# Kernel optimization log

Measured on AMD Instinct MI355X. Metric: run time of the kernel, lower is better.

Reference implementation:

```python
import jax, jax.numpy as jnp
import numpy as np
import math

BS, QLEN, DIM, NHEADS = 2, 2048, 1024, 16
HEAD = DIM // NHEADS

def linear(x, w, b):
    # torch nn.Linear: y = x @ w.T + b, w: [out, in]
    return x @ w.T + b

def setup_inputs() -> dict:
    key = jax.random.key(0)
    ks = jax.random.split(key, 6)
    s = 1.0 / math.sqrt(DIM)
    return {
        "input": jax.random.normal(ks[0], (BS * QLEN, DIM), jnp.float32),
        "mask": jnp.zeros((BS, 1, 1, QLEN), jnp.float32),
        "q_w": jax.random.normal(ks[1], (DIM, DIM), jnp.float32) * s,
        "q_b": jnp.zeros((DIM,), jnp.float32),
        "k_w": jax.random.normal(ks[2], (DIM, DIM), jnp.float32) * s,
        "k_b": jnp.zeros((DIM,), jnp.float32),
        "v_w": jax.random.normal(ks[3], (DIM, DIM), jnp.float32) * s,
        "v_b": jnp.zeros((DIM,), jnp.float32),
        "o_w": jax.random.normal(ks[4], (DIM, DIM), jnp.float32) * s,
        "o_b": jnp.zeros((DIM,), jnp.float32),
        "bs": BS,
        "qlen": QLEN,
    }

def reference(input, mask, q_w, q_b, k_w, k_b, v_w, v_b, o_w, o_b, bs, qlen):
    dim = input.shape[-1]
    n_heads = NHEADS
    dph = dim // n_heads

    def split_heads(x):  # [bs*qlen, dim] -> [bs, h, qlen, dph]
        return x.reshape(bs, qlen, n_heads, dph).transpose(0, 2, 1, 3)

    q = split_heads(linear(input, q_w, q_b)) * (1.0 / math.sqrt(dph))
    k = split_heads(linear(input, k_w, k_b))
    v = split_heads(linear(input, v_w, v_b))

    scores = jnp.einsum('bhqd,bhkd->bhqk', q, k) + mask
    weights = jax.nn.softmax(scores.astype(jnp.float32), axis=-1).astype(scores.dtype)
    # dropout: eval mode (training=False) -> identity
    context = jnp.einsum('bhqk,bhkd->bhqd', weights, v)
    context = context.transpose(0, 2, 1, 3).reshape(bs * qlen, dim)
    return linear(context, o_w, o_b)
```

## Files before the change

### kernel.cpp

```cpp
#include <hip/hip_runtime.h>
#include <hip/hip_bf16.h>

typedef __bf16 bf16;
typedef __attribute__((ext_vector_type(8))) __bf16 bf16x8;
typedef __attribute__((ext_vector_type(4))) __bf16 bf16x4;
typedef __attribute__((ext_vector_type(4))) float f32x4;

#define GLOAD_LDS16(g, l) __builtin_amdgcn_global_load_lds( \
    (const __attribute__((address_space(1))) void*)(g),     \
    (__attribute__((address_space(3))) void*)(l), 16, 0, 0)

#if __has_builtin(__builtin_amdgcn_exp2f)
#define EXP2F(x) __builtin_amdgcn_exp2f(x)
#else
#define EXP2F(x) exp2f(x)
#endif

constexpr int MTOT = 4096;
constexpr int DIMC = 1024;
constexpr int QL   = 2048;
constexpr int NH   = 16;
constexpr int HD   = 64;
constexpr float LOG2E = 1.44269504088896340736f;

__global__ __launch_bounds__(256) void prep_cvt(
    const float* __restrict__ x,  const float* __restrict__ qw,
    const float* __restrict__ kw, const float* __restrict__ vw,
    const float* __restrict__ ow, const float* __restrict__ mask,
    bf16* __restrict__ Xb, bf16* __restrict__ Wq, bf16* __restrict__ Wk,
    bf16* __restrict__ Wv, bf16* __restrict__ Wo, bf16* __restrict__ Mexp)
{
  const long long bid = blockIdx.x;
  if (bid >= 8192) {
    const int off = (int)(bid - 8192) * 1024 + threadIdx.x * 4;
    float4 f = *reinterpret_cast<const float4*>(mask + off);
    bf16x4 v;
    v[0] = (bf16)exp2f(f.x * LOG2E); v[1] = (bf16)exp2f(f.y * LOG2E);
    v[2] = (bf16)exp2f(f.z * LOG2E); v[3] = (bf16)exp2f(f.w * LOG2E);
    *reinterpret_cast<bf16x4*>(Mexp + off) = v;
    return;
  }
  const long long i = (bid * 256 + threadIdx.x) * 4;
  const long long nX = (long long)MTOT * DIMC;
  const long long nW = (long long)DIMC * DIMC;
  const float* src; bf16* dst; long long off;
  if      (i < nX)          { src = x;  dst = Xb; off = i; }
  else if (i < nX + nW)     { src = qw; dst = Wq; off = i - nX; }
  else if (i < nX + 2*nW)   { src = kw; dst = Wk; off = i - nX - nW; }
  else if (i < nX + 3*nW)   { src = vw; dst = Wv; off = i - nX - 2*nW; }
  else                      { src = ow; dst = Wo; off = i - nX - 3*nW; }
  float4 f = *reinterpret_cast<const float4*>(src + off);
  bf16x4 v;
  v[0] = (bf16)f.x; v[1] = (bf16)f.y; v[2] = (bf16)f.z; v[3] = (bf16)f.w;
  *reinterpret_cast<bf16x4*>(dst + off) = v;
}

__global__ __launch_bounds__(128, 2) void gemm_bt(
    const bf16* __restrict__ A,
    const bf16* __restrict__ W0, const bf16* __restrict__ W1, const bf16* __restrict__ W2,
    const float* __restrict__ b0, const float* __restrict__ b1, const float* __restrict__ b2,
    bf16* __restrict__ D0, bf16* __restrict__ D1,
    bf16* __restrict__ VtOut, const bf16* __restrict__ Mexp, float scale0)
{
  __shared__ __align__(16) bf16 SMEM[16384];
  bf16* As = SMEM;
  bf16* Bs = SMEM + 8192;

  const bf16* Bm; const float* bias; bf16* D = nullptr; float scale = 1.f;
  const int z = blockIdx.z;
  if (z == 0)      { Bm = W0; bias = b0; D = D0; scale = scale0; }
  else if (z == 1) { Bm = W1; bias = b1; D = D1; }
  else             { Bm = W2; bias = b2; }

  const int tid  = threadIdx.x;
  const int w    = tid >> 6, lane = tid & 63;
  const int gm0  = blockIdx.x * 128, gn0 = blockIdx.y * 128;
  const int wc   = w * 64;
  const int lr   = lane & 15;
  const int lkB  = (lane >> 4) * 16;
  const int srow = (w << 3) + (lane >> 3);
  const int scolE = (((lane & 7) * 16) ^ (((lane >> 3) & 7) << 4)) >> 1;

  f32x4 acc[8][4] = {};

  for (int kt = 0; kt < DIMC / 64; ++kt) {
    __syncthreads();
    const int k0 = kt * 64;
#pragma unroll
    for (int p = 0; p < 8; ++p) {
      const int r = p * 16 + srow;
      GLOAD_LDS16(A  + (size_t)(gm0 + r) * DIMC + k0 + scolE, &As[(p * 16 + (w << 3)) * 64]);
      GLOAD_LDS16(Bm + (size_t)(gn0 + r) * DIMC + k0 + scolE, &Bs[(p * 16 + (w << 3)) * 64]);
    }
    asm volatile("s_waitcnt vmcnt(0)" ::: "memory");
    __syncthreads();

#pragma unroll
    for (int kk = 0; kk < 2; ++kk) {
      bf16x8 af[8], bfv[4];
#pragma unroll
      for (int mf = 0; mf < 8; ++mf) {
        const int r = mf * 16 + lr;
        const int cE = ((kk * 64 + lkB) ^ ((r & 7) << 4)) >> 1;
        af[mf] = *reinterpret_cast<const bf16x8*>(&As[r * 64 + cE]);
      }
#pragma unroll
      for (int nf = 0; nf < 4; ++nf) {
        const int r = wc + nf * 16 + lr;
        const int cE = ((kk * 64 + lkB) ^ ((r & 7) << 4)) >> 1;
        bfv[nf] = *reinterpret_cast<const bf16x8*>(&Bs[r * 64 + cE]);
      }
#pragma unroll
      for (int mf = 0; mf < 8; ++mf)
#pragma unroll
        for (int nf = 0; nf < 4; ++nf)
          acc[mf][nf] = __builtin_amdgcn_mfma_f32_16x16x32_bf16(af[mf], bfv[nf], acc[mf][nf], 0, 0, 0);
    }
  }

  const int orow = (lane >> 4) * 4;

  if (z == 2) {
    bf16* T = SMEM;
    __syncthreads();
#pragma unroll
    for (int mf = 0; mf < 8; ++mf) {
#pragma unroll
      for (int nf = 0; nf < 4; ++nf) {
        const int cl = wc + nf * 16 + lr;
        const float bv = bias[gn0 + cl];
        const int xx = (cl & 7) << 3;
        const int rl0 = mf * 16 + orow;
        bf16x4 tv;
#pragma unroll
        for (int i = 0; i < 4; ++i) tv[i] = (bf16)(acc[mf][nf][i] + bv);
        *reinterpret_cast<bf16x4*>(&T[cl * 128 + (rl0 ^ xx)]) = tv;
      }
    }
    __syncthreads();
    const int c   = tid;
    const int xx2 = (c & 7) << 3;
    const int cg  = gn0 + c;
    const int bb  = gm0 >> 11;
    const int kvb = gm0 & 2047;
    bf16* vtrow = VtOut + (((size_t)bb * 16 + (cg >> 6)) * 64 + (cg & 63)) * (size_t)QL
                  + kvb;
    const bf16* mrow = Mexp + (size_t)bb * QL + kvb;
    const int st = c & 15;
#pragma unroll
    for (int j = 0; j < 16; ++j) {
      const int jj = (j + st) & 15;
      bf16x8 vv = *reinterpret_cast<const bf16x8*>(&T[c * 128 + ((jj * 8) ^ xx2)]);
      const bf16x8 me = *reinterpret_cast<const bf16x8*>(mrow + jj * 8);
#pragma unroll
      for (int e = 0; e < 8; ++e) vv[e] = (bf16)((float)vv[e] * (float)me[e]);
      *reinterpret_cast<bf16x8*>(vtrow + jj * 8) = vv;
    }
    return;
  }

#pragma unroll
  for (int mf = 0; mf < 8; ++mf) {
#pragma unroll
    for (int nf = 0; nf < 4; ++nf) {
      const int c = gn0 + wc + nf * 16 + lr;
      const float bv = bias[c];
#pragma unroll
      for (int i = 0; i < 4; ++i) {
        const int r = gm0 + mf * 16 + orow + i;
        D[(size_t)r * DIMC + c] = (bf16)((acc[mf][nf][i] + bv) * scale);
      }
    }
  }
}

__global__ __launch_bounds__(256) void gemm_o(
    const bf16* __restrict__ A, const bf16* __restrict__ W,
    const float* __restrict__ bias, float* __restrict__ out)
{
  __shared__ __align__(16) bf16 As[128 * 64];
  __shared__ __align__(16) bf16 Bs[64 * 64];

  const int tid  = threadIdx.x;
  const int w    = tid >> 6, lane = tid & 63;
  const int gm0  = blockIdx.x * 128, gn0 = blockIdx.y * 64;
  const int wr   = (w >> 1) * 64, wc = (w & 1) * 32;
  const int lr   = lane & 15;
  const int lkB  = (lane >> 4) * 16;
  const int srow = (w << 3) + (lane >> 3);
  const int scolE = (((lane & 7) * 16) ^ ((lane >> 3) << 4)) >> 1;

  f32x4 acc[4][2] = {};

  for (int kt = 0; kt < DIMC / 64; ++kt) {
    __syncthreads();
    const int k0 = kt * 64;
#pragma unroll
    for (int p = 0; p < 4; ++p) {
      const int r = p * 32 + srow;
      GLOAD_LDS16(A + (size_t)(gm0 + r) * DIMC + k0 + scolE, &As[(p * 32 + (w << 3)) * 64]);
    }
#pragma unroll
    for (int p = 0; p < 2; ++p) {
      const int r = p * 32 + srow;
      GLOAD_LDS16(W + (size_t)(gn0 + r) * DIMC + k0 + scolE, &Bs[(p * 32 + (w << 3)) * 64]);
    }
    asm volatile("s_waitcnt vmcnt(0)" ::: "memory");
    __syncthreads();

#pragma unroll
    for (int kk = 0; kk < 2; ++kk) {
      bf16x8 af[4], bfv[2];
#pragma unroll
      for (int mf = 0; mf < 4; ++mf) {
        const int r = wr + mf * 16 + lr;
        const int cE = ((kk * 64 + lkB) ^ ((r & 7) << 4)) >> 1;
        af[mf] = *reinterpret_cast<const bf16x8*>(&As[r * 64 + cE]);
      }
#pragma unroll
      for (int nf = 0; nf < 2; ++nf) {
        const int r = wc + nf * 16 + lr;
        const int cE = ((kk * 64 + lkB) ^ ((r & 7) << 4)) >> 1;
        bfv[nf] = *reinterpret_cast<const bf16x8*>(&Bs[r * 64 + cE]);
      }
#pragma unroll
      for (int mf = 0; mf < 4; ++mf)
#pragma unroll
        for (int nf = 0; nf < 2; ++nf)
          acc[mf][nf] = __builtin_amdgcn_mfma_f32_16x16x32_bf16(af[mf], bfv[nf], acc[mf][nf], 0, 0, 0);
    }
  }

  const int orow = (lane >> 4) * 4;
#pragma unroll
  for (int mf = 0; mf < 4; ++mf) {
#pragma unroll
    for (int nf = 0; nf < 2; ++nf) {
      const int c = gn0 + wc + nf * 16 + lr;
      const float bv = bias[c];
#pragma unroll
      for (int i = 0; i < 4; ++i) {
        const int r = gm0 + wr + mf * 16 + orow + i;
        out[(size_t)r * DIMC + c] = acc[mf][nf][i] + bv;
      }
    }
  }
}

__global__ __launch_bounds__(256, 2) void attn_fwd(
    const bf16* __restrict__ Q, const bf16* __restrict__ K, const bf16* __restrict__ Vt,
    const bf16* __restrict__ Mexp, bf16* __restrict__ ctx)
{
  __shared__ __align__(16) bf16 Kls[4 * 4096];
  __shared__ __align__(16) bf16 Vls[4 * 4096];
  __shared__ __align__(16) bf16 Ps[4][2 * 16 * 36];

  const int tid = threadIdx.x, w = tid >> 6, lane = tid & 63;
  const int bid = blockIdx.x;
  const int logical = (bid & 7) * 64 + (bid >> 3);
  const int qt = logical & 15, bh = logical >> 4;
  const int b = bh >> 4, h = bh & 15;
  const size_t rowbase = (size_t)b * QL;
  const int lr = lane & 15, g = lane >> 4;
  const int lkB = g * 16;

  bf16x8 aq[2][2];
#pragma unroll
  for (int s = 0; s < 2; ++s) {
    const bf16* qp = Q + (rowbase + qt * 128 + w * 32 + s * 16 + lr) * DIMC + h * HD + g * 8;
    aq[s][0] = *reinterpret_cast<const bf16x8*>(qp);
    aq[s][1] = *reinterpret_cast<const bf16x8*>(qp + 32);
  }

  int g_row[2], g_colE[2];
#pragma unroll
  for (int s2 = 0; s2 < 2; ++s2) {
    const int ci = s2 * 256 + tid;
    const int row = ci >> 3;
    g_row[s2]  = row;
    g_colE[s2] = (((ci & 7) * 16) ^ ((row & 7) << 4)) >> 1;
  }
  const bf16* Kt0 = K  + rowbase * DIMC + h * HD;
  const bf16* Vt0 = Vt + (size_t)bh * HD * QL;
  const bf16* MexpP = Mexp + rowbase;

#define ATTN_STAGE(tt, bb) do {                                               \
    _Pragma("unroll")                                                         \
    for (int s2 = 0; s2 < 2; ++s2) {                                          \
      GLOAD_LDS16(Kt0 + (size_t)((tt) * 64 + g_row[s2]) * DIMC + g_colE[s2],  \
                  &Kls[(bb) * 4096 + (s2 * 256 + tid) * 8]);                  \
      GLOAD_LDS16(Vt0 + (size_t)g_row[s2] * QL + (tt) * 64 + g_colE[s2],      \
                  &Vls[(bb) * 4096 + (s2 * 256 + tid) * 8]);                  \
    }                                                                         \
  } while (0)

  const f32x4 zf4 = {0.f, 0.f, 0.f, 0.f};

#define QK_COMPUTE(TT, SACC) do {                                             \
    const bf16* Kb = &Kls[((TT) & 3) * 4096];                                 \
    bf16x8 bk0[4], bk1[4];                                                    \
    _Pragma("unroll")                                                         \
    for (int nf = 0; nf < 4; ++nf) {                                          \
      const int r = nf * 16 + lr;                                             \
      const int c0 = ((lkB)      ^ ((r & 7) << 4)) >> 1;                      \
      const int c1 = ((64 + lkB) ^ ((r & 7) << 4)) >> 1;                      \
      bk0[nf] = *reinterpret_cast<const bf16x8*>(&Kb[r * 64 + c0]);           \
      bk1[nf] = *reinterpret_cast<const bf16x8*>(&Kb[r * 64 + c1]);           \
    }                                                                         \
    __builtin_amdgcn_s_setprio(1);                                            \
    _Pragma("unroll")                                                         \
    for (int s = 0; s < 2; ++s)                                               \
      _Pragma("unroll")                                                       \
      for (int nf = 0; nf < 4; ++nf)                                          \
        SACC[s][nf] = __builtin_amdgcn_mfma_f32_16x16x32_bf16(bk0[nf], aq[s][0], zf4, 0, 0, 0); \
    _Pragma("unroll")                                                         \
    for (int s = 0; s < 2; ++s)                                               \
      _Pragma("unroll")                                                       \
      for (int nf = 0; nf < 4; ++nf)                                          \
        SACC[s][nf] = __builtin_amdgcn_mfma_f32_16x16x32_bf16(bk1[nf], aq[s][1], SACC[s][nf], 0, 0, 0); \
    __builtin_amdgcn_s_setprio(0);                                            \
  } while (0)

#define SM_PV_HALF(TT, SC, HALF) do {                                         \
    _Pragma("unroll")                                                         \
    for (int s = 0; s < 2; ++s) {                                             \
      _Pragma("unroll")                                                       \
      for (int nn = 0; nn < 2; ++nn) {                                        \
        const int nf = (HALF) * 2 + nn;                                       \
        const float p0 = EXP2F(SC[s][nf][0]);                                 \
        const float p1 = EXP2F(SC[s][nf][1]);                                 \
        const float p2 = EXP2F(SC[s][nf][2]);                                 \
        const float p3 = EXP2F(SC[s][nf][3]);                                 \
        bf16x4 pv;                                                            \
        pv[0] = (bf16)p0; pv[1] = (bf16)p1; pv[2] = (bf16)p2; pv[3] = (bf16)p3; \
        *reinterpret_cast<bf16x4*>(&Ps[w][s * 576 + lr * 36 + nn * 16 + g * 4]) = pv; \
      }                                                                       \
    }                                                                         \
    const bf16x8 mfrag = *reinterpret_cast<const bf16x8*>(                    \
        MexpP + (TT) * 64 + (HALF) * 32 + g * 8);                             \
    const bf16* Vb = &Vls[((TT) & 3) * 4096];                                 \
    bf16x8 bv[4];                                                             \
    _Pragma("unroll")                                                         \
    for (int df = 0; df < 4; ++df) {                                          \
      const int r = df * 16 + lr;                                             \
      const int cE = (((HALF) * 64 + lkB) ^ ((r & 7) << 4)) >> 1;             \
      bv[df] = *reinterpret_cast<const bf16x8*>(&Vb[r * 64 + cE]);            \
    }                                                                         \
    bf16x8 ap0, ap1;                                                          \
    {                                                                         \
      const bf16x4 lo0 = *reinterpret_cast<const bf16x4*>(&Ps[w][0 * 576 + lr * 36 + g * 8]); \
      const bf16x4 hi0 = *reinterpret_cast<const bf16x4*>(&Ps[w][0 * 576 + lr * 36 + g * 8 + 4]); \
      const bf16x4 lo1 = *reinterpret_cast<const bf16x4*>(&Ps[w][1 * 576 + lr * 36 + g * 8]); \
      const bf16x4 hi1 = *reinterpret_cast<const bf16x4*>(&Ps[w][1 * 576 + lr * 36 + g * 8 + 4]); \
      _Pragma("unroll")                                                       \
      for (int j = 0; j < 4; ++j) {                                           \
        ap0[j] = lo0[j]; ap0[4 + j] = hi0[j];                                 \
        ap1[j] = lo1[j]; ap1[4 + j] = hi1[j];                                 \
      }                                                                       \
    }                                                                         \
    __builtin_amdgcn_s_setprio(1);                                            \
    acc_l[0] = __builtin_amdgcn_mfma_f32_16x16x32_bf16(ap0, mfrag, acc_l[0], 0, 0, 0); \
    acc_l[1] = __builtin_amdgcn_mfma_f32_16x16x32_bf16(ap1, mfrag, acc_l[1], 0, 0, 0); \
    _Pragma("unroll")                                                         \
    for (int df = 0; df < 4; ++df)                                            \
      acc_o[0][df] = __builtin_amdgcn_mfma_f32_16x16x32_bf16(ap0, bv[df], acc_o[0][df], 0, 0, 0); \
    _Pragma("unroll")                                                         \
    for (int df = 0; df < 4; ++df)                                            \
      acc_o[1][df] = __builtin_amdgcn_mfma_f32_16x16x32_bf16(ap1, bv[df], acc_o[1][df], 0, 0, 0); \
    __builtin_amdgcn_s_setprio(0);                                            \
  } while (0)

#define ITER_END() do {                                                       \
    asm volatile("s_waitcnt vmcnt(4) lgkmcnt(0)" ::: "memory");               \
    __builtin_amdgcn_s_barrier();                                             \
    __builtin_amdgcn_sched_barrier(0);                                        \
  } while (0)

  f32x4 acc_l[2] = {};
  f32x4 acc_o[2][4] = {};
  f32x4 sA[2][4], sB[2][4];

  constexpr int NT = QL / 64;

  ATTN_STAGE(0, 0);
  ATTN_STAGE(1, 1);
  ATTN_STAGE(2, 2);
  asm volatile("s_waitcnt vmcnt(8)" ::: "memory");
  __builtin_amdgcn_s_barrier();
  QK_COMPUTE(0, sA);
  ITER_END();

  for (int tt = 0; tt < NT; tt += 2) {
    {
      const int T = tt;
      const int stg = (T + 3 < NT) ? (T + 3) : (NT - 1);
      ATTN_STAGE(stg, (T + 3) & 3);
      QK_COMPUTE(T + 1, sB);
      SM_PV_HALF(T, sA, 0);
      SM_PV_HALF(T, sA, 1);
      ITER_END();
    }
    {
      const int T = tt + 1;
      const int stg = (T + 3 < NT) ? (T + 3) : (NT - 1);
      ATTN_STAGE(stg, (T + 3) & 3);
      if (T + 1 < NT) QK_COMPUTE(T + 1, sA);
      SM_PV_HALF(T, sB, 0);
      SM_PV_HALF(T, sB, 1);
      ITER_END();
    }
  }
#undef ATTN_STAGE
#undef QK_COMPUTE
#undef SM_PV_HALF
#undef ITER_END

#pragma unroll
  for (int s = 0; s < 2; ++s) {
#pragma unroll
    for (int i = 0; i < 4; ++i) {
      const float inv = 1.0f / acc_l[s][i];
      const size_t r = rowbase + qt * 128 + w * 32 + s * 16 + g * 4 + i;
#pragma unroll
      for (int df = 0; df < 4; ++df)
        ctx[r * DIMC + h * HD + df * 16 + lr] = (bf16)(acc_o[s][df][i] * inv);
    }
  }
}

extern "C" void kernel_launch(void* const* d_in, const int* in_sizes, int n_in,
                              void* d_out, int out_size, void* d_ws, size_t ws_size,
                              hipStream_t stream) {
  const float* x    = (const float*)d_in[0];
  const float* mask = (const float*)d_in[1];
  const float* qw = (const float*)d_in[2]; const float* qb = (const float*)d_in[3];
  const float* kw = (const float*)d_in[4]; const float* kb = (const float*)d_in[5];
  const float* vw = (const float*)d_in[6]; const float* vb = (const float*)d_in[7];
  const float* ow = (const float*)d_in[8]; const float* ob = (const float*)d_in[9];
  float* out = (float*)d_out;

  bf16* Xb  = (bf16*)d_ws;
  bf16* Wqb = Xb  + (size_t)MTOT * DIMC;
  bf16* Wkb = Wqb + (size_t)DIMC * DIMC;
  bf16* Wvb = Wkb + (size_t)DIMC * DIMC;
  bf16* Wob = Wvb + (size_t)DIMC * DIMC;
  bf16* Qb  = Wob + (size_t)DIMC * DIMC;
  bf16* Kb  = Qb  + (size_t)MTOT * DIMC;
  bf16* Cb  = Kb  + (size_t)MTOT * DIMC;
  bf16* Vt  = Cb  + (size_t)MTOT * DIMC;
  bf16* Mex = Vt  + (size_t)MTOT * DIMC;

  prep_cvt<<<8196, 256, 0, stream>>>(x, qw, kw, vw, ow, mask,
                                     Xb, Wqb, Wkb, Wvb, Wob, Mex);

  gemm_bt<<<dim3(32, 8, 3), 128, 0, stream>>>(
      Xb, Wqb, Wkb, Wvb, qb, kb, vb, Qb, Kb, Vt, Mex, 0.125f * LOG2E);

  attn_fwd<<<512, 256, 0, stream>>>(Qb, Kb, Vt, Mex, Cb);

  gemm_o<<<dim3(32, 16), 256, 0, stream>>>(Cb, Wob, ob, out);
}
```

Baseline: 106.7 us.

## Double-buffer LDS tiles in projection GEMMs to overlap loads with MFMA

Both projection GEMM kernels now keep two shared-memory stages. The next K tile is issued with global_load_lds before the current tile is computed, and a single wait plus barrier sits at the end of each iteration. This is meant to hide global-memory latency behind the matrix instructions, and s_setprio raises wave priority around the MFMA block. The cost is more LDS per block: 64KB for gemm_bt and 48KB for gemm_o. That may lower occupancy, notably for gemm_bt with launch bounds of 2 blocks per CU.

```diff
diff --git a/kernel.cpp b/kernel.cpp
--- a/kernel.cpp
+++ b/kernel.cpp
@@ -62,9 +62,7 @@
     bf16* __restrict__ D0, bf16* __restrict__ D1,
     bf16* __restrict__ VtOut, const bf16* __restrict__ Mexp, float scale0)
 {
-  __shared__ __align__(16) bf16 SMEM[16384];
-  bf16* As = SMEM;
-  bf16* Bs = SMEM + 8192;
+  __shared__ __align__(16) bf16 SMEM[32768];
 
   const bf16* Bm; const float* bias; bf16* D = nullptr; float scale = 1.f;
   const int z = blockIdx.z;
@@ -81,19 +79,29 @@
   const int srow = (w << 3) + (lane >> 3);
   const int scolE = (((lane & 7) * 16) ^ (((lane >> 3) & 7) << 4)) >> 1;
 
+#define G_STAGE(kt, bb) do {                                                  \
+    const int k0_ = (kt) * 64;                                                \
+    bf16* As_ = SMEM + (bb) * 16384;                                          \
+    bf16* Bs_ = As_ + 8192;                                                   \
+    _Pragma("unroll")                                                         \
+    for (int p = 0; p < 8; ++p) {                                             \
+      const int r = p * 16 + srow;                                            \
+      GLOAD_LDS16(A  + (size_t)(gm0 + r) * DIMC + k0_ + scolE, &As_[(p * 16 + (w << 3)) * 64]); \
+      GLOAD_LDS16(Bm + (size_t)(gn0 + r) * DIMC + k0_ + scolE, &Bs_[(p * 16 + (w << 3)) * 64]); \
+    }                                                                         \
+  } while (0)
+
   f32x4 acc[8][4] = {};
 
+  G_STAGE(0, 0);
+  asm volatile("s_waitcnt vmcnt(0)" ::: "memory");
+  __builtin_amdgcn_s_barrier();
+
+  int buf = 0;
   for (int kt = 0; kt < DIMC / 64; ++kt) {
-    __syncthreads();
-    const int k0 = kt * 64;
-#pragma unroll
-    for (int p = 0; p < 8; ++p) {
-      const int r = p * 16 + srow;
-      GLOAD_LDS16(A  + (size_t)(gm0 + r) * DIMC + k0 + scolE, &As[(p * 16 + (w << 3)) * 64]);
-      GLOAD_LDS16(Bm + (size_t)(gn0 + r) * DIMC + k0 + scolE, &Bs[(p * 16 + (w << 3)) * 64]);
-    }
-    asm volatile("s_waitcnt vmcnt(0)" ::: "memory");
-    __syncthreads();
+    if (kt < DIMC / 64 - 1) G_STAGE(kt + 1, buf ^ 1);
+    const bf16* As_ = SMEM + buf * 16384;
+    const bf16* Bs_ = As_ + 8192;
 
 #pragma unroll
     for (int kk = 0; kk < 2; ++kk) {
@@ -102,21 +110,29 @@
       for (int mf = 0; mf < 8; ++mf) {
         const int r = mf * 16 + lr;
         const int cE = ((kk * 64 + lkB) ^ ((r & 7) << 4)) >> 1;
-        af[mf] = *reinterpret_cast<const bf16x8*>(&As[r * 64 + cE]);
+        af[mf] = *reinterpret_cast<const bf16x8*>(&As_[r * 64 + cE]);
       }
 #pragma unroll
       for (int nf = 0; nf < 4; ++nf) {
         const int r = wc + nf * 16 + lr;
         const int cE = ((kk * 64 + lkB) ^ ((r & 7) << 4)) >> 1;
-        bfv[nf] = *reinterpret_cast<const bf16x8*>(&Bs[r * 64 + cE]);
-      }
+        bfv[nf] = *reinterpret_cast<const bf16x8*>(&Bs_[r * 64 + cE]);
+      }
+      __builtin_amdgcn_s_setprio(1);
 #pragma unroll
       for (int mf = 0; mf < 8; ++mf)
 #pragma unroll
         for (int nf = 0; nf < 4; ++nf)
           acc[mf][nf] = __builtin_amdgcn_mfma_f32_16x16x32_bf16(af[mf], bfv[nf], acc[mf][nf], 0, 0, 0);
-    }
-  }
+      __builtin_amdgcn_s_setprio(0);
+    }
+
+    asm volatile("s_waitcnt vmcnt(0) lgkmcnt(0)" ::: "memory");
+    __builtin_amdgcn_s_barrier();
+    __builtin_amdgcn_sched_barrier(0);
+    buf ^= 1;
+  }
+#undef G_STAGE
 
   const int orow = (lane >> 4) * 4;
 
@@ -178,8 +194,7 @@
     const bf16* __restrict__ A, const bf16* __restrict__ W,
     const float* __restrict__ bias, float* __restrict__ out)
 {
-  __shared__ __align__(16) bf16 As[128 * 64];
-  __shared__ __align__(16) bf16 Bs[64 * 64];
+  __shared__ __align__(16) bf16 SMEM[24576];
 
   const int tid  = threadIdx.x;
   const int w    = tid >> 6, lane = tid & 63;
@@ -190,23 +205,33 @@
   const int srow = (w << 3) + (lane >> 3);
   const int scolE = (((lane & 7) * 16) ^ ((lane >> 3) << 4)) >> 1;
 
+#define O_STAGE(kt, bb) do {                                                  \
+    const int k0_ = (kt) * 64;                                                \
+    bf16* As_ = SMEM + (bb) * 12288;                                          \
+    bf16* Bs_ = As_ + 8192;                                                   \
+    _Pragma("unroll")                                                         \
+    for (int p = 0; p < 4; ++p) {                                             \
+      const int r = p * 32 + srow;                                            \
+      GLOAD_LDS16(A + (size_t)(gm0 + r) * DIMC + k0_ + scolE, &As_[(p * 32 + (w << 3)) * 64]); \
+    }                                                                         \
+    _Pragma("unroll")                                                         \
+    for (int p = 0; p < 2; ++p) {                                             \
+      const int r = p * 32 + srow;                                            \
+      GLOAD_LDS16(W + (size_t)(gn0 + r) * DIMC + k0_ + scolE, &Bs_[(p * 32 + (w << 3)) * 64]); \
+    }                                                                         \
+  } while (0)
+
   f32x4 acc[4][2] = {};
 
+  O_STAGE(0, 0);
+  asm volatile("s_waitcnt vmcnt(0)" ::: "memory");
+  __builtin_amdgcn_s_barrier();
+
+  int buf = 0;
   for (int kt = 0; kt < DIMC / 64; ++kt) {
-    __syncthreads();
-    const int k0 = kt * 64;
-#pragma unroll
-    for (int p = 0; p < 4; ++p) {
-      const int r = p * 32 + srow;
-      GLOAD_LDS16(A + (size_t)(gm0 + r) * DIMC + k0 + scolE, &As[(p * 32 + (w << 3)) * 64]);
-    }
-#pragma unroll
-    for (int p = 0; p < 2; ++p) {
-      const int r = p * 32 + srow;
-      GLOAD_LDS16(W + (size_t)(gn0 + r) * DIMC + k0 + scolE, &Bs[(p * 32 + (w << 3)) * 64]);
-    }
-    asm volatile("s_waitcnt vmcnt(0)" ::: "memory");
-    __syncthreads();
+    if (kt < DIMC / 64 - 1) O_STAGE(kt + 1, buf ^ 1);
+    const bf16* As_ = SMEM + buf * 12288;
+    const bf16* Bs_ = As_ + 8192;
 
 #pragma unroll
     for (int kk = 0; kk < 2; ++kk) {
@@ -215,21 +240,29 @@
       for (int mf = 0; mf < 4; ++mf) {
         const int r = wr + mf * 16 + lr;
         const int cE = ((kk * 64 + lkB) ^ ((r & 7) << 4)) >> 1;
-        af[mf] = *reinterpret_cast<const bf16x8*>(&As[r * 64 + cE]);
+        af[mf] = *reinterpret_cast<const bf16x8*>(&As_[r * 64 + cE]);
       }
 #pragma unroll
       for (int nf = 0; nf < 2; ++nf) {
         const int r = wc + nf * 16 + lr;
         const int cE = ((kk * 64 + lkB) ^ ((r & 7) << 4)) >> 1;
-        bfv[nf] = *reinterpret_cast<const bf16x8*>(&Bs[r * 64 + cE]);
-      }
+        bfv[nf] = *reinterpret_cast<const bf16x8*>(&Bs_[r * 64 + cE]);
+      }
+      __builtin_amdgcn_s_setprio(1);
 #pragma unroll
       for (int mf = 0; mf < 4; ++mf)
 #pragma unroll
         for (int nf = 0; nf < 2; ++nf)
           acc[mf][nf] = __builtin_amdgcn_mfma_f32_16x16x32_bf16(af[mf], bfv[nf], acc[mf][nf], 0, 0, 0);
-    }
-  }
+      __builtin_amdgcn_s_setprio(0);
+    }
+
+    asm volatile("s_waitcnt vmcnt(0) lgkmcnt(0)" ::: "memory");
+    __builtin_amdgcn_s_barrier();
+    __builtin_amdgcn_sched_barrier(0);
+    buf ^= 1;
+  }
+#undef O_STAGE
 
   const int orow = (lane >> 4) * 4;
 #pragma unroll
```

New measurement: 120.7 us. 13.2% more time.

## Process attention KV tiles in pairs with one barrier per pair

Applied to the files above, without the earlier changes.

Restructures the flash-attention main loop so that two KV tiles are staged, QK-computed and softmax/PV-processed together, with a single full wait and barrier per pair instead of per tile. The prefetch distance drops from three tiles ahead to two, and the barrier now waits for vmcnt(0). This cuts barrier count and allows interleaving of two QK products, but weakens the overlap of global loads with compute. Prefetching still happens at pair granularity.

```diff
diff --git a/kernel.cpp b/kernel.cpp
--- a/kernel.cpp
+++ b/kernel.cpp
@@ -370,8 +370,8 @@
     __builtin_amdgcn_s_setprio(0);                                            \
   } while (0)
 
-#define ITER_END() do {                                                       \
-    asm volatile("s_waitcnt vmcnt(4) lgkmcnt(0)" ::: "memory");               \
+#define PAIR_END() do {                                                       \
+    asm volatile("s_waitcnt vmcnt(0) lgkmcnt(0)" ::: "memory");               \
     __builtin_amdgcn_s_barrier();                                             \
     __builtin_amdgcn_sched_barrier(0);                                        \
   } while (0)
@@ -384,36 +384,29 @@
 
   ATTN_STAGE(0, 0);
   ATTN_STAGE(1, 1);
-  ATTN_STAGE(2, 2);
-  asm volatile("s_waitcnt vmcnt(8)" ::: "memory");
+  asm volatile("s_waitcnt vmcnt(0)" ::: "memory");
   __builtin_amdgcn_s_barrier();
-  QK_COMPUTE(0, sA);
-  ITER_END();
-
-  for (int tt = 0; tt < NT; tt += 2) {
-    {
-      const int T = tt;
-      const int stg = (T + 3 < NT) ? (T + 3) : (NT - 1);
-      ATTN_STAGE(stg, (T + 3) & 3);
-      QK_COMPUTE(T + 1, sB);
-      SM_PV_HALF(T, sA, 0);
-      SM_PV_HALF(T, sA, 1);
-      ITER_END();
-    }
-    {
-      const int T = tt + 1;
-      const int stg = (T + 3 < NT) ? (T + 3) : (NT - 1);
-      ATTN_STAGE(stg, (T + 3) & 3);
-      if (T + 1 < NT) QK_COMPUTE(T + 1, sA);
-      SM_PV_HALF(T, sB, 0);
-      SM_PV_HALF(T, sB, 1);
-      ITER_END();
-    }
+
+  for (int p = 0; p < NT / 2; ++p) {
+    const int T0 = 2 * p, T1 = 2 * p + 1;
+    const int s0 = (T0 + 2 < NT) ? T0 + 2 : NT - 2;
+    const int s1 = (T1 + 2 < NT) ? T1 + 2 : NT - 1;
+    ATTN_STAGE(s0, (T0 + 2) & 3);
+    ATTN_STAGE(s1, (T1 + 2) & 3);
+
+    QK_COMPUTE(T0, sA);
+    QK_COMPUTE(T1, sB);
+    SM_PV_HALF(T0, sA, 0);
+    SM_PV_HALF(T0, sA, 1);
+    SM_PV_HALF(T1, sB, 0);
+    SM_PV_HALF(T1, sB, 1);
+
+    PAIR_END();
   }
 #undef ATTN_STAGE
 #undef QK_COMPUTE
 #undef SM_PV_HALF
-#undef ITER_END
+#undef PAIR_END
 
 #pragma unroll
   for (int s = 0; s < 2; ++s) {
```

New measurement: 103.4 us. -3.0%, faster.
